# Performance work log

Measured on AMD Instinct MI355X. Metric: run time of the kernel, lower is better.

## Reference

```python
import jax, jax.numpy as jnp
import numpy as np

K = 64          # num_clusters
S = 4           # num_shadow
DIM = 128
ALPHA = 100.0
EPS = 1e-12     # F.normalize eps


def setup_inputs() -> dict:
    key = jax.random.key(0)
    k1, k2 = jax.random.split(key)
    x = jax.random.normal(k1, (16, DIM, 30, 40), dtype=jnp.float32)
    centroids = jax.random.uniform(k2, (K, S + 1, DIM), dtype=jnp.float32)
    return {"x": x, "centroids": centroids}


def reference(x, centroids):
    N, C, H, W = x.shape
    P = H * W
    # conv weight/bias derived from centroids (as in _init_params)
    c_flat = centroids.reshape(K * (S + 1), C)                      # (M, C)
    w = 2.0 * ALPHA * c_flat                                        # (M, C)
    b = -ALPHA * jnp.linalg.norm(c_flat, axis=1)                    # (M,)
    xf = x.reshape(N, C, P)                                         # (N, C, P)
    # 1x1 conv == per-pixel matmul
    conv_out = jnp.einsum('ncp,mc->nmp', xf, w) + b[None, :, None]
    conv_out = conv_out.reshape(N, K, S + 1, P)
    # dual softmax: over clusters (axis=1) and over shadows (axis=2)
    soft_assign = jax.nn.softmax(conv_out, axis=1) * jax.nn.softmax(conv_out, axis=2)
    # loop `residual += sa_i * residual` == residual0 * prod_i(1 + sa_i)
    mult = jnp.prod(1.0 + soft_assign, axis=2)                      # (N, K, P)
    rep = centroids[:, 0, :]                                        # (K, C) representative centroids
    # sum_p mult * (x - rep) without materializing (N,K,C,P)
    out = jnp.einsum('ncp,nkp->nkc', xf, mult) \
          - rep[None, :, :] * jnp.sum(mult, axis=-1)[:, :, None]    # (N, K, C)
    # intra-cluster L2 norm (per descriptor dim)
    out = out / jnp.maximum(jnp.linalg.norm(out, axis=2, keepdims=True), EPS)
    out = out.reshape(N, -1)
    # global L2 norm
    out = out / jnp.maximum(jnp.linalg.norm(out, axis=1, keepdims=True), EPS)
    return out
```

## Files before the change

kernel.cpp:

```cpp
#include <hip/hip_runtime.h>
#include <math.h>

typedef _Float16 f16;
typedef unsigned short u16;
typedef unsigned int u32;
typedef f16 f16x8 __attribute__((ext_vector_type(8)));
typedef float f32x4 __attribute__((ext_vector_type(4)));

namespace {
constexpr int Kc  = 64;
constexpr int SP1 = 5;
constexpr int Mm  = Kc * SP1;
constexpr int DIM = 128;
constexpr int Nn  = 16;
constexpr int Pp  = 1200;
constexpr int PT  = 64;
constexpr int NT  = (Pp + PT - 1) / PT;
constexpr int WAVES = 16;
constexpr int TPB   = WAVES * 64;
constexpr int KPW   = Kc / WAVES;

constexpr int OFF_A    = 0;
constexpr int OFF_BH   = 87040;
constexpr int OFF_BL   = 104448;
constexpr int OFF_PART = 121856;
constexpr int OFF_M1F  = 142336;
constexpr int OFF_Z1F  = 143616;
constexpr int OFF_MS   = 144896;
constexpr int OFF_BS   = 154112;
constexpr int LDS_TOTAL = 155392;
}

__global__ __launch_bounds__(1024) void k_prep(
    const float* __restrict__ cent, float* __restrict__ b,
    u16* __restrict__ Ah, u16* __restrict__ Al) {
  const int w = threadIdx.x >> 6, lane = threadIdx.x & 63;
  const int m = blockIdx.x * 16 + w;
  const float v0 = cent[(size_t)m * DIM + lane];
  const float v1 = cent[(size_t)m * DIM + 64 + lane];
  float s = v0 * v0 + v1 * v1;
  #pragma unroll
  for (int off = 32; off > 0; off >>= 1) s += __shfl_down(s, off, 64);
  if (lane == 0) b[m] = -100.0f * sqrtf(s);
  const f16 h0 = (f16)v0, h1 = (f16)v1;
  Ah[(size_t)m * DIM + lane]      = __builtin_bit_cast(u16, h0);
  Ah[(size_t)m * DIM + 64 + lane] = __builtin_bit_cast(u16, h1);
  Al[(size_t)m * DIM + lane]      = __builtin_bit_cast(u16, (f16)(v0 - (float)h0));
  Al[(size_t)m * DIM + 64 + lane] = __builtin_bit_cast(u16, (f16)(v1 - (float)h1));
}

__global__ __launch_bounds__(TPB, 4) void k_fused(
    const float* __restrict__ x, const u16* __restrict__ Ah_g,
    const u16* __restrict__ Al_g, const float* __restrict__ b_g,
    float* __restrict__ out_part, float* __restrict__ S_part) {
  const int tile = blockIdx.x, n = blockIdx.y;
  const int p0 = tile * PT, cnt = min(PT, Pp - p0);
  const int t = threadIdx.x, lane = t & 63, w = t >> 6;
  const int l15 = lane & 15, g = lane >> 4;
  const bool act = lane < cnt;

  extern __shared__ __align__(16) char smem[];
  f16*   Ablk    = (f16*)(smem + OFF_A);
  u32*   Ablk32  = (u32*)(smem + OFF_A);
  f16*   Bh_s    = (f16*)(smem + OFF_BH);
  u32*   Bh32    = (u32*)(smem + OFF_BH);
  f16*   Bl_s    = (f16*)(smem + OFF_BL);
  u32*   Bl32    = (u32*)(smem + OFF_BL);
  float* part    = (float*)(smem + OFF_PART);
  float* scratch = (float*)(smem + OFF_PART);
  float* m1f     = (float*)(smem + OFF_M1F);
  float* z1f     = (float*)(smem + OFF_Z1F);
  f16*   mult_s  = (f16*)(smem + OFF_MS);
  float* b_s     = (float*)(smem + OFF_BS);
  float* convs   = (float*)(smem + OFF_A);
  u16*   xpv     = (u16*)(smem + OFF_A);

  for (int i2 = t; i2 < Mm * DIM / 2; i2 += TPB) {
    const int m = i2 >> 6, c2 = i2 & 63;
    Ablk32[m * 68 + c2] = ((const u32*)Ah_g)[i2];
  }
  for (int i = t; i < DIM * PT; i += TPB) {
    const int c = i >> 6, p = i & 63;
    scratch[p * 129 + c] = (p < cnt) ? x[((size_t)n * DIM + c) * Pp + p0 + p] : 0.f;
  }
  __syncthreads();

  for (int i = t; i < PT * 64; i += TPB) {
    const int p = i >> 6, c2 = i & 63;
    const float v0 = scratch[p * 129 + 2 * c2];
    const float v1 = scratch[p * 129 + 2 * c2 + 1];
    const f16 h0 = (f16)v0, h1 = (f16)v1;
    const f16 l0 = (f16)(v0 - (float)h0), l1 = (f16)(v1 - (float)h1);
    Bh32[p * 68 + c2] = (u32)__builtin_bit_cast(u16, h0) |
                        ((u32)__builtin_bit_cast(u16, h1) << 16);
    Bl32[p * 68 + c2] = (u32)__builtin_bit_cast(u16, l0) |
                        ((u32)__builtin_bit_cast(u16, l1) << 16);
  }
  __syncthreads();

  const int wm = w >> 2, wp = w & 3;
  const int m0 = wm * 80;
  f32x4 acc[5];
  #pragma unroll
  for (int i = 0; i < 5; ++i) acc[i] = (f32x4){0.f, 0.f, 0.f, 0.f};

  #pragma unroll
  for (int seg = 0; seg < 3; ++seg) {
    if (seg == 2) {
      __syncthreads();
      for (int i2 = t; i2 < Mm * DIM / 2; i2 += TPB) {
        const int m = i2 >> 6, c2 = i2 & 63;
        Ablk32[m * 68 + c2] = ((const u32*)Al_g)[i2];
      }
      if (t < Mm) b_s[t] = b_g[t];
      __syncthreads();
    }
    const f16* Bseg = (seg == 1) ? Bl_s : Bh_s;
    #pragma unroll
    for (int kc = 0; kc < 4; ++kc) {
      const f16x8 bf = *(const f16x8*)&Bseg[(wp * 16 + l15) * 136 + kc * 32 + g * 8];
      #pragma unroll
      for (int t5 = 0; t5 < 5; ++t5) {
        const f16x8 af = *(const f16x8*)&Ablk[(m0 + t5 * 16 + l15) * 136 + kc * 32 + g * 8];
        acc[t5] = __builtin_amdgcn_mfma_f32_16x16x32_f16(af, bf, acc[t5], 0, 0, 0);
      }
    }
  }
  __syncthreads();

  const int pcol = wp * 16 + l15;
  #pragma unroll
  for (int t5 = 0; t5 < 5; ++t5)
    #pragma unroll
    for (int r = 0; r < 4; ++r) {
      const int m = m0 + t5 * 16 + g * 4 + r;
      convs[m * 64 + pcol] = fmaf(200.0f, acc[t5][r], b_s[m]);
    }
  __syncthreads();

  float cv[KPW][SP1];
  float m1loc[SP1];
  #pragma unroll
  for (int s = 0; s < SP1; ++s) m1loc[s] = -3.4e38f;
  #pragma unroll
  for (int kk = 0; kk < KPW; ++kk)
    #pragma unroll
    for (int s = 0; s < SP1; ++s) {
      const float v = convs[((w * KPW + kk) * SP1 + s) * 64 + lane];
      cv[kk][s] = v;
      m1loc[s] = fmaxf(m1loc[s], v);
    }
  __syncthreads();

  for (int i = t; i < DIM * PT; i += TPB) {
    const int c = i >> 6, p = i & 63;
    xpv[c * 72 + p] = ((const u16*)Bh_s)[p * 136 + c];
  }

  #pragma unroll
  for (int s = 0; s < SP1; ++s) part[(w * SP1 + s) * 64 + lane] = m1loc[s];
  __syncthreads();
  if (t < SP1 * 64) {
    const int s = t >> 6, l = t & 63;
    float m = part[s * 64 + l];
    #pragma unroll
    for (int ww = 1; ww < WAVES; ++ww) m = fmaxf(m, part[(ww * SP1 + s) * 64 + l]);
    m1f[s * 64 + l] = m;
  }
  __syncthreads();
  float m1r[SP1];
  #pragma unroll
  for (int s = 0; s < SP1; ++s) m1r[s] = m1f[s * 64 + lane];
  float z1loc[SP1] = {0.f, 0.f, 0.f, 0.f, 0.f};
  #pragma unroll
  for (int kk = 0; kk < KPW; ++kk)
    #pragma unroll
    for (int s = 0; s < SP1; ++s) z1loc[s] += __expf(cv[kk][s] - m1r[s]);
  #pragma unroll
  for (int s = 0; s < SP1; ++s) part[(w * SP1 + s) * 64 + lane] = z1loc[s];
  __syncthreads();
  if (t < SP1 * 64) {
    const int s = t >> 6, l = t & 63;
    float z = part[s * 64 + l];
    #pragma unroll
    for (int ww = 1; ww < WAVES; ++ww) z += part[(ww * SP1 + s) * 64 + l];
    z1f[s * 64 + l] = z;
  }
  __syncthreads();
  float z1r[SP1];
  #pragma unroll
  for (int s = 0; s < SP1; ++s) z1r[s] = z1f[s * 64 + lane];

  #pragma unroll
  for (int kk = 0; kk < KPW; ++kk) {
    const int k = w * KPW + kk;
    float M2 = cv[kk][0];
    #pragma unroll
    for (int s = 1; s < SP1; ++s) M2 = fmaxf(M2, cv[kk][s]);
    float e2[SP1], Z2 = 0.f;
    #pragma unroll
    for (int s = 0; s < SP1; ++s) { e2[s] = __expf(cv[kk][s] - M2); Z2 += e2[s]; }
    float mlt = 1.f;
    #pragma unroll
    for (int s = 0; s < SP1; ++s) {
      const float e1 = __expf(cv[kk][s] - m1r[s]);
      mlt *= 1.f + (e1 / z1r[s]) * (e2[s] / Z2);
    }
    mult_s[k * 72 + lane] = act ? (f16)mlt : (f16)0.f;
    float msum = act ? mlt : 0.f;
    #pragma unroll
    for (int off = 32; off > 0; off >>= 1) msum += __shfl_down(msum, off, 64);
    if (lane == 0) S_part[((size_t)n * NT + tile) * Kc + k] = msum;
  }
  __syncthreads();

  const int wm2 = w & 3;
  const int wn2 = (w >> 2) * 2;
  f32x4 acc2[2];
  acc2[0] = (f32x4){0.f, 0.f, 0.f, 0.f};
  acc2[1] = (f32x4){0.f, 0.f, 0.f, 0.f};
  #pragma unroll
  for (int kc = 0; kc < 2; ++kc) {
    const f16x8 am = *(const f16x8*)&mult_s[(wm2 * 16 + l15) * 72 + kc * 32 + g * 8];
    #pragma unroll
    for (int tn = 0; tn < 2; ++tn) {
      const f16x8 bx = *(const f16x8*)((const f16*)xpv + ((wn2 + tn) * 16 + l15) * 72 + kc * 32 + g * 8);
      acc2[tn] = __builtin_amdgcn_mfma_f32_16x16x32_f16(am, bx, acc2[tn], 0, 0, 0);
    }
  }
  float* dst = out_part + ((size_t)(n * NT + tile) * Kc) * DIM;
  #pragma unroll
  for (int tn = 0; tn < 2; ++tn)
    #pragma unroll
    for (int r = 0; r < 4; ++r)
      dst[(wm2 * 16 + g * 4 + r) * DIM + (wn2 + tn) * 16 + l15] = acc2[tn][r];
}

__global__ __launch_bounds__(256) void k_norm(
    const float* __restrict__ out_part, const float* __restrict__ cent,
    const float* __restrict__ S_part, float* __restrict__ out) {
  const int n = blockIdx.y, k0 = blockIdx.x * 4;
  __shared__ float Sk[4];
  if (threadIdx.x < 4) {
    float s = 0.f;
    for (int tt = 0; tt < NT; ++tt)
      s += S_part[((size_t)n * NT + tt) * Kc + k0 + threadIdx.x];
    Sk[threadIdx.x] = s;
  }
  __syncthreads();
  const int kl = threadIdx.x >> 6, cl = threadIdx.x & 63;
  const int k = k0 + kl;
  const float sk = Sk[kl];
  float v[2], ss = 0.f;
  #pragma unroll
  for (int j = 0; j < 2; ++j) {
    const int c = cl + 64 * j;
    float a = 0.f;
    for (int tt = 0; tt < NT; ++tt)
      a += out_part[(((size_t)n * NT + tt) * Kc + k) * DIM + c];
    v[j] = a - cent[(size_t)k * SP1 * DIM + c] * sk;
    ss = fmaf(v[j], v[j], ss);
  }
  #pragma unroll
  for (int off = 32; off > 0; off >>= 1) ss += __shfl_xor(ss, off, 64);
  const float kinv = 0.125f / fmaxf(sqrtf(ss), 1e-12f);
  #pragma unroll
  for (int j = 0; j < 2; ++j)
    out[((size_t)n * Kc + k) * DIM + cl + 64 * j] = v[j] * kinv;
}

extern "C" void kernel_launch(void* const* d_in, const int* in_sizes, int n_in,
                              void* d_out, int out_size, void* d_ws, size_t ws_size,
                              hipStream_t stream) {
  const float* x    = (const float*)d_in[0];
  const float* cent = (const float*)d_in[1];
  float* out = (float*)d_out;

  float* b        = (float*)d_ws;
  float* S_part   = b + 384;
  float* out_part = S_part + (size_t)Nn * NT * Kc;
  u16* Ah_g = (u16*)(out_part + (size_t)Nn * NT * Kc * DIM);
  u16* Al_g = Ah_g + (size_t)Mm * DIM;

  k_prep<<<dim3(Mm / 16), dim3(1024), 0, stream>>>(cent, b, Ah_g, Al_g);
  k_fused<<<dim3(NT, Nn), dim3(TPB), LDS_TOTAL, stream>>>(
      x, Ah_g, Al_g, b, out_part, S_part);
  k_norm<<<dim3(Kc / 4, Nn), dim3(256), 0, stream>>>(out_part, cent, S_part, out);
}
```

Measured before the change: 117.0 us.

## Shrink fused block to 512 threads, read centroid fragments from global, process tile in halves

The fused kernel now uses 512 threads and about 64KB of static LDS instead of 1024 threads and 155KB of dynamic LDS. It no longer stages the split-f16 centroid matrices in LDS; MFMA A fragments are loaded directly from global memory, where the small matrices should stay in cache. Each 64-pixel tile is handled as two 32-pixel halves, with the second matmul accumulating across halves and cross-half reductions done via shuffles. The aim is higher occupancy and less LDS fill work, at the cost of repeated global/L2 loads for A fragments and extra synchronisation per half.

```diff
diff --git a/kernel.cpp b/kernel.cpp
--- a/kernel.cpp
+++ b/kernel.cpp
@@ -10,25 +10,24 @@
 namespace {
 constexpr int Kc  = 64;
 constexpr int SP1 = 5;
-constexpr int Mm  = Kc * SP1;
+constexpr int Mm  = 320;
 constexpr int DIM = 128;
 constexpr int Nn  = 16;
 constexpr int Pp  = 1200;
-constexpr int PT  = 64;
-constexpr int NT  = (Pp + PT - 1) / PT;
-constexpr int WAVES = 16;
-constexpr int TPB   = WAVES * 64;
-constexpr int KPW   = Kc / WAVES;
-
-constexpr int OFF_A    = 0;
-constexpr int OFF_BH   = 87040;
-constexpr int OFF_BL   = 104448;
-constexpr int OFF_PART = 121856;
-constexpr int OFF_M1F  = 142336;
-constexpr int OFF_Z1F  = 143616;
-constexpr int OFF_MS   = 144896;
-constexpr int OFF_BS   = 154112;
-constexpr int LDS_TOTAL = 155392;
+constexpr int PT  = 32;
+constexpr int NT  = 19;
+constexpr int TPB = 512;
+
+constexpr int OFF_BH   = 0;
+constexpr int OFF_BL   = 8704;
+constexpr int OFF_CV   = 17408;
+constexpr int OFF_PART = 17408;
+constexpr int OFF_M1F  = 22528;
+constexpr int OFF_Z1F  = 23168;
+constexpr int OFF_MS   = 23808;
+constexpr int OFF_XPV  = 28928;
+constexpr int OFF_BS   = 63488;
+constexpr int LDS_TOTAL = 64768;
 }
 
 __global__ __launch_bounds__(1024) void k_prep(
@@ -54,186 +53,194 @@
     const u16* __restrict__ Al_g, const float* __restrict__ b_g,
     float* __restrict__ out_part, float* __restrict__ S_part) {
   const int tile = blockIdx.x, n = blockIdx.y;
-  const int p0 = tile * PT, cnt = min(PT, Pp - p0);
   const int t = threadIdx.x, lane = t & 63, w = t >> 6;
   const int l15 = lane & 15, g = lane >> 4;
-  const bool act = lane < cnt;
-
-  extern __shared__ __align__(16) char smem[];
-  f16*   Ablk    = (f16*)(smem + OFF_A);
-  u32*   Ablk32  = (u32*)(smem + OFF_A);
-  f16*   Bh_s    = (f16*)(smem + OFF_BH);
+  const int pp = t & 31, kgrp = t >> 5;
+
+  __shared__ __align__(16) char smem[LDS_TOTAL];
+  f16*   Bh      = (f16*)(smem + OFF_BH);
   u32*   Bh32    = (u32*)(smem + OFF_BH);
-  f16*   Bl_s    = (f16*)(smem + OFF_BL);
+  u16*   BhU     = (u16*)(smem + OFF_BH);
+  f16*   Bl      = (f16*)(smem + OFF_BL);
   u32*   Bl32    = (u32*)(smem + OFF_BL);
+  float* convs   = (float*)(smem + OFF_CV);
+  float* scratch = (float*)(smem + OFF_CV);
   float* part    = (float*)(smem + OFF_PART);
-  float* scratch = (float*)(smem + OFF_PART);
   float* m1f     = (float*)(smem + OFF_M1F);
   float* z1f     = (float*)(smem + OFF_Z1F);
-  f16*   mult_s  = (f16*)(smem + OFF_MS);
+  f16*   ms      = (f16*)(smem + OFF_MS);
+  f16*   xpv     = (f16*)(smem + OFF_XPV);
   float* b_s     = (float*)(smem + OFF_BS);
-  float* convs   = (float*)(smem + OFF_A);
-  u16*   xpv     = (u16*)(smem + OFF_A);
-
-  for (int i2 = t; i2 < Mm * DIM / 2; i2 += TPB) {
-    const int m = i2 >> 6, c2 = i2 & 63;
-    Ablk32[m * 68 + c2] = ((const u32*)Ah_g)[i2];
-  }
-  for (int i = t; i < DIM * PT; i += TPB) {
-    const int c = i >> 6, p = i & 63;
-    scratch[p * 129 + c] = (p < cnt) ? x[((size_t)n * DIM + c) * Pp + p0 + p] : 0.f;
-  }
-  __syncthreads();
-
-  for (int i = t; i < PT * 64; i += TPB) {
-    const int p = i >> 6, c2 = i & 63;
-    const float v0 = scratch[p * 129 + 2 * c2];
-    const float v1 = scratch[p * 129 + 2 * c2 + 1];
-    const f16 h0 = (f16)v0, h1 = (f16)v1;
-    const f16 l0 = (f16)(v0 - (float)h0), l1 = (f16)(v1 - (float)h1);
-    Bh32[p * 68 + c2] = (u32)__builtin_bit_cast(u16, h0) |
-                        ((u32)__builtin_bit_cast(u16, h1) << 16);
-    Bl32[p * 68 + c2] = (u32)__builtin_bit_cast(u16, l0) |
-                        ((u32)__builtin_bit_cast(u16, l1) << 16);
-  }
-  __syncthreads();
-
-  const int wm = w >> 2, wp = w & 3;
+
+  if (t < Mm) b_s[t] = b_g[t];
+
+  const int wm = w >> 1, wp = w & 1;
   const int m0 = wm * 80;
-  f32x4 acc[5];
-  #pragma unroll
-  for (int i = 0; i < 5; ++i) acc[i] = (f32x4){0.f, 0.f, 0.f, 0.f};
-
-  #pragma unroll
-  for (int seg = 0; seg < 3; ++seg) {
-    if (seg == 2) {
-      __syncthreads();
-      for (int i2 = t; i2 < Mm * DIM / 2; i2 += TPB) {
-        const int m = i2 >> 6, c2 = i2 & 63;
-        Ablk32[m * 68 + c2] = ((const u32*)Al_g)[i2];
-      }
-      if (t < Mm) b_s[t] = b_g[t];
-      __syncthreads();
-    }
-    const f16* Bseg = (seg == 1) ? Bl_s : Bh_s;
-    #pragma unroll
-    for (int kc = 0; kc < 4; ++kc) {
-      const f16x8 bf = *(const f16x8*)&Bseg[(wp * 16 + l15) * 136 + kc * 32 + g * 8];
-      #pragma unroll
-      for (int t5 = 0; t5 < 5; ++t5) {
-        const f16x8 af = *(const f16x8*)&Ablk[(m0 + t5 * 16 + l15) * 136 + kc * 32 + g * 8];
-        acc[t5] = __builtin_amdgcn_mfma_f32_16x16x32_f16(af, bf, acc[t5], 0, 0, 0);
-      }
-    }
-  }
-  __syncthreads();
-
-  const int pcol = wp * 16 + l15;
-  #pragma unroll
-  for (int t5 = 0; t5 < 5; ++t5)
-    #pragma unroll
-    for (int r = 0; r < 4; ++r) {
-      const int m = m0 + t5 * 16 + g * 4 + r;
-      convs[m * 64 + pcol] = fmaf(200.0f, acc[t5][r], b_s[m]);
-    }
-  __syncthreads();
-
-  float cv[KPW][SP1];
-  float m1loc[SP1];
-  #pragma unroll
-  for (int s = 0; s < SP1; ++s) m1loc[s] = -3.4e38f;
-  #pragma unroll
-  for (int kk = 0; kk < KPW; ++kk)
-    #pragma unroll
-    for (int s = 0; s < SP1; ++s) {
-      const float v = convs[((w * KPW + kk) * SP1 + s) * 64 + lane];
-      cv[kk][s] = v;
-      m1loc[s] = fmaxf(m1loc[s], v);
-    }
-  __syncthreads();
-
-  for (int i = t; i < DIM * PT; i += TPB) {
-    const int c = i >> 6, p = i & 63;
-    xpv[c * 72 + p] = ((const u16*)Bh_s)[p * 136 + c];
-  }
-
-  #pragma unroll
-  for (int s = 0; s < SP1; ++s) part[(w * SP1 + s) * 64 + lane] = m1loc[s];
-  __syncthreads();
-  if (t < SP1 * 64) {
-    const int s = t >> 6, l = t & 63;
-    float m = part[s * 64 + l];
-    #pragma unroll
-    for (int ww = 1; ww < WAVES; ++ww) m = fmaxf(m, part[(ww * SP1 + s) * 64 + l]);
-    m1f[s * 64 + l] = m;
-  }
-  __syncthreads();
-  float m1r[SP1];
-  #pragma unroll
-  for (int s = 0; s < SP1; ++s) m1r[s] = m1f[s * 64 + lane];
-  float z1loc[SP1] = {0.f, 0.f, 0.f, 0.f, 0.f};
-  #pragma unroll
-  for (int kk = 0; kk < KPW; ++kk)
-    #pragma unroll
-    for (int s = 0; s < SP1; ++s) z1loc[s] += __expf(cv[kk][s] - m1r[s]);
-  #pragma unroll
-  for (int s = 0; s < SP1; ++s) part[(w * SP1 + s) * 64 + lane] = z1loc[s];
-  __syncthreads();
-  if (t < SP1 * 64) {
-    const int s = t >> 6, l = t & 63;
-    float z = part[s * 64 + l];
-    #pragma unroll
-    for (int ww = 1; ww < WAVES; ++ww) z += part[(ww * SP1 + s) * 64 + l];
-    z1f[s * 64 + l] = z;
-  }
-  __syncthreads();
-  float z1r[SP1];
-  #pragma unroll
-  for (int s = 0; s < SP1; ++s) z1r[s] = z1f[s * 64 + lane];
-
-  #pragma unroll
-  for (int kk = 0; kk < KPW; ++kk) {
-    const int k = w * KPW + kk;
-    float M2 = cv[kk][0];
-    #pragma unroll
-    for (int s = 1; s < SP1; ++s) M2 = fmaxf(M2, cv[kk][s]);
-    float e2[SP1], Z2 = 0.f;
-    #pragma unroll
-    for (int s = 0; s < SP1; ++s) { e2[s] = __expf(cv[kk][s] - M2); Z2 += e2[s]; }
-    float mlt = 1.f;
-    #pragma unroll
-    for (int s = 0; s < SP1; ++s) {
-      const float e1 = __expf(cv[kk][s] - m1r[s]);
-      mlt *= 1.f + (e1 / z1r[s]) * (e2[s] / Z2);
-    }
-    mult_s[k * 72 + lane] = act ? (f16)mlt : (f16)0.f;
-    float msum = act ? mlt : 0.f;
-    #pragma unroll
-    for (int off = 32; off > 0; off >>= 1) msum += __shfl_down(msum, off, 64);
-    if (lane == 0) S_part[((size_t)n * NT + tile) * Kc + k] = msum;
-  }
-  __syncthreads();
-
-  const int wm2 = w & 3;
-  const int wn2 = (w >> 2) * 2;
-  f32x4 acc2[2];
-  acc2[0] = (f32x4){0.f, 0.f, 0.f, 0.f};
-  acc2[1] = (f32x4){0.f, 0.f, 0.f, 0.f};
-  #pragma unroll
-  for (int kc = 0; kc < 2; ++kc) {
-    const f16x8 am = *(const f16x8*)&mult_s[(wm2 * 16 + l15) * 72 + kc * 32 + g * 8];
-    #pragma unroll
-    for (int tn = 0; tn < 2; ++tn) {
-      const f16x8 bx = *(const f16x8*)((const f16*)xpv + ((wn2 + tn) * 16 + l15) * 72 + kc * 32 + g * 8);
+  const int ktile = w & 3, cbase = (w >> 2) * 4;
+
+  f32x4 acc2[4];
+  #pragma unroll
+  for (int i = 0; i < 4; ++i) acc2[i] = (f32x4){0.f, 0.f, 0.f, 0.f};
+  float msum4[4] = {0.f, 0.f, 0.f, 0.f};
+
+  for (int half = 0; half < 2; ++half) {
+    const int p0 = tile * 64 + half * 32;
+    const int cnt = min(PT, Pp - p0);
+
+    __syncthreads();
+
+    for (int i = t; i < PT * DIM; i += TPB) {
+      const int c = i >> 5, p = i & 31;
+      scratch[p * 132 + c] = (p < cnt) ? x[((size_t)n * DIM + c) * Pp + p0 + p] : 0.f;
+    }
+    __syncthreads();
+    for (int i = t; i < PT * 64; i += TPB) {
+      const int p = i >> 6, c2 = i & 63;
+      const float v0 = scratch[p * 132 + 2 * c2];
+      const float v1 = scratch[p * 132 + 2 * c2 + 1];
+      const f16 h0 = (f16)v0, h1 = (f16)v1;
+      const f16 l0 = (f16)(v0 - (float)h0), l1 = (f16)(v1 - (float)h1);
+      Bh32[p * 68 + c2] = (u32)__builtin_bit_cast(u16, h0) |
+                          ((u32)__builtin_bit_cast(u16, h1) << 16);
+      Bl32[p * 68 + c2] = (u32)__builtin_bit_cast(u16, l0) |
+                          ((u32)__builtin_bit_cast(u16, l1) << 16);
+    }
+    __syncthreads();
+
+    f32x4 acc[5];
+    #pragma unroll
+    for (int i = 0; i < 5; ++i) acc[i] = (f32x4){0.f, 0.f, 0.f, 0.f};
+    #pragma unroll
+    for (int seg = 0; seg < 3; ++seg) {
+      const u16* Aseg = (seg == 2) ? Al_g : Ah_g;
+      const f16* Bseg = (seg == 1) ? Bl : Bh;
+      #pragma unroll
+      for (int kc = 0; kc < 4; ++kc) {
+        const f16x8 bf = *(const f16x8*)&Bseg[(wp * 16 + l15) * 136 + kc * 32 + g * 8];
+        #pragma unroll
+        for (int t5 = 0; t5 < 5; ++t5) {
+          const f16x8 af = *(const f16x8*)(Aseg +
+              (size_t)(m0 + t5 * 16 + l15) * 128 + kc * 32 + g * 8);
+          acc[t5] = __builtin_amdgcn_mfma_f32_16x16x32_f16(af, bf, acc[t5], 0, 0, 0);
+        }
+      }
+    }
+    const int pcol = wp * 16 + l15;
+    #pragma unroll
+    for (int t5 = 0; t5 < 5; ++t5)
+      #pragma unroll
+      for (int r = 0; r < 4; ++r) {
+        const int m = m0 + t5 * 16 + g * 4 + r;
+        convs[m * 36 + pcol] = fmaf(200.0f, acc[t5][r], b_s[m]);
+      }
+    __syncthreads();
+
+    float cv[4][SP1], m1loc[SP1];
+    #pragma unroll
+    for (int s = 0; s < SP1; ++s) m1loc[s] = -3.4e38f;
+    #pragma unroll
+    for (int kk = 0; kk < 4; ++kk) {
+      const int k = kgrp * 4 + kk;
+      #pragma unroll
+      for (int s = 0; s < SP1; ++s) {
+        const float v = convs[(k * SP1 + s) * 36 + pp];
+        cv[kk][s] = v;
+        m1loc[s] = fmaxf(m1loc[s], v);
+      }
+    }
+    __syncthreads();
+
+    for (int i = t; i < DIM * PT; i += TPB) {
+      const int c = i >> 5, p = i & 31;
+      ((u16*)xpv)[c * 40 + p] = BhU[p * 136 + c];
+    }
+
+    #pragma unroll
+    for (int s = 0; s < SP1; ++s)
+      m1loc[s] = fmaxf(m1loc[s], __shfl_xor(m1loc[s], 32, 64));
+    if (lane < 32) {
+      #pragma unroll
+      for (int s = 0; s < SP1; ++s) part[(w * SP1 + s) * 32 + pp] = m1loc[s];
+    }
+    __syncthreads();
+    if (t < SP1 * 32) {
+      const int s = t >> 5, l = t & 31;
+      float m = part[s * 32 + l];
+      #pragma unroll
+      for (int ww = 1; ww < 8; ++ww) m = fmaxf(m, part[(ww * SP1 + s) * 32 + l]);
+      m1f[s * 32 + l] = m;
+    }
+    __syncthreads();
+    float m1r[SP1];
+    #pragma unroll
+    for (int s = 0; s < SP1; ++s) m1r[s] = m1f[s * 32 + pp];
+    float z1loc[SP1] = {0.f, 0.f, 0.f, 0.f, 0.f};
+    #pragma unroll
+    for (int kk = 0; kk < 4; ++kk)
+      #pragma unroll
+      for (int s = 0; s < SP1; ++s) z1loc[s] += __expf(cv[kk][s] - m1r[s]);
+    #pragma unroll
+    for (int s = 0; s < SP1; ++s) z1loc[s] += __shfl_xor(z1loc[s], 32, 64);
+    if (lane < 32) {
+      #pragma unroll
+      for (int s = 0; s < SP1; ++s) part[(w * SP1 + s) * 32 + pp] = z1loc[s];
+    }
+    __syncthreads();
+    if (t < SP1 * 32) {
+      const int s = t >> 5, l = t & 31;
+      float z = part[s * 32 + l];
+      #pragma unroll
+      for (int ww = 1; ww < 8; ++ww) z += part[(ww * SP1 + s) * 32 + l];
+      z1f[s * 32 + l] = z;
+    }
+    __syncthreads();
+    float z1r[SP1];
+    #pragma unroll
+    for (int s = 0; s < SP1; ++s) z1r[s] = z1f[s * 32 + pp];
+
+    const bool act = pp < cnt;
+    #pragma unroll
+    for (int kk = 0; kk < 4; ++kk) {
+      const int k = kgrp * 4 + kk;
+      float M2 = cv[kk][0];
+      #pragma unroll
+      for (int s = 1; s < SP1; ++s) M2 = fmaxf(M2, cv[kk][s]);
+      float e2[SP1], Z2 = 0.f;
+      #pragma unroll
+      for (int s = 0; s < SP1; ++s) { e2[s] = __expf(cv[kk][s] - M2); Z2 += e2[s]; }
+      float mlt = 1.f;
+      #pragma unroll
+      for (int s = 0; s < SP1; ++s) {
+        const float e1 = __expf(cv[kk][s] - m1r[s]);
+        mlt *= 1.f + (e1 / z1r[s]) * (e2[s] / Z2);
+      }
+      ms[k * 40 + pp] = act ? (f16)mlt : (f16)0.f;
+      float msum = act ? mlt : 0.f;
+      #pragma unroll
+      for (int off = 16; off > 0; off >>= 1) msum += __shfl_down(msum, off, 32);
+      msum4[kk] += msum;
+    }
+    __syncthreads();
+
+    const f16x8 am = *(const f16x8*)&ms[(ktile * 16 + l15) * 40 + g * 8];
+    #pragma unroll
+    for (int tn = 0; tn < 4; ++tn) {
+      const f16x8 bx = *(const f16x8*)&xpv[((cbase + tn) * 16 + l15) * 40 + g * 8];
       acc2[tn] = __builtin_amdgcn_mfma_f32_16x16x32_f16(am, bx, acc2[tn], 0, 0, 0);
     }
   }
+
   float* dst = out_part + ((size_t)(n * NT + tile) * Kc) * DIM;
   #pragma unroll
-  for (int tn = 0; tn < 2; ++tn)
+  for (int tn = 0; tn < 4; ++tn)
     #pragma unroll
     for (int r = 0; r < 4; ++r)
-      dst[(wm2 * 16 + g * 4 + r) * DIM + (wn2 + tn) * 16 + l15] = acc2[tn][r];
+      dst[(ktile * 16 + g * 4 + r) * DIM + (cbase + tn) * 16 + l15] = acc2[tn][r];
+  if (pp == 0) {
+    #pragma unroll
+    for (int kk = 0; kk < 4; ++kk)
+      S_part[((size_t)n * NT + tile) * Kc + kgrp * 4 + kk] = msum4[kk];
+  }
 }
 
 __global__ __launch_bounds__(256) void k_norm(
@@ -283,7 +290,7 @@
   u16* Al_g = Ah_g + (size_t)Mm * DIM;
 
   k_prep<<<dim3(Mm / 16), dim3(1024), 0, stream>>>(cent, b, Ah_g, Al_g);
-  k_fused<<<dim3(NT, Nn), dim3(TPB), LDS_TOTAL, stream>>>(
+  k_fused<<<dim3(NT, Nn), dim3(TPB), 0, stream>>>(
       x, Ah_g, Al_g, b, out_part, S_part);
   k_norm<<<dim3(Kc / 4, Nn), dim3(256), 0, stream>>>(out_part, cent, S_part, out);
 }
```

Result: slower. 213.7 us (+82.6%).
